# Performance work log

Hardware: AMD Instinct MI355X
Metric: run time of the kernel (lower is better)

The kernel has to match this reference:

```python
import jax, jax.numpy as jnp
import numpy as np

NUM_GRAPHS = 512
N_NODES = 100000
N_EDGES = 1600000
D_NODE = 128
D_EDGE = 32
D_OUT = 64


def setup_inputs() -> dict:
    key = jax.random.key(0)
    k = jax.random.split(key, 6)
    x = jax.random.normal(k[0], (N_NODES, D_NODE), dtype=jnp.float32)
    edge_index = jax.random.randint(k[1], (2, N_EDGES), 0, N_NODES, dtype=jnp.int64)
    edge_attr = jax.random.normal(k[2], (N_EDGES, D_EDGE), dtype=jnp.float32)
    u = jax.random.normal(k[3], (NUM_GRAPHS, D_OUT), dtype=jnp.float32)
    batch = jnp.sort(jax.random.randint(k[4], (N_NODES,), 0, NUM_GRAPHS, dtype=jnp.int64))
    W = jax.random.normal(k[5], (D_NODE + D_EDGE, D_OUT), dtype=jnp.float32) * 0.05
    b = jnp.full((D_OUT,), 0.01, dtype=jnp.float32)
    return {"x": x, "edge_index": edge_index, "edge_attr": edge_attr, "u": u, "batch": batch, "W": W, "b": b}


def reference(x, edge_index, edge_attr, u, batch, W, b):
    # row, col = edge_index; only col is used
    col = edge_index[1]
    # scatter_add nodes by graph id -> [B, D_NODE]
    node_aggregate = jax.ops.segment_sum(x, batch, num_segments=NUM_GRAPHS)
    # scatter_add edges by graph id of target node -> [B, D_EDGE]
    edge_aggregate = jax.ops.segment_sum(edge_attr, batch[col], num_segments=NUM_GRAPHS)
    out = jnp.concatenate([node_aggregate, edge_aggregate], axis=1)  # [B, 160]
    return out @ W + b  # [B, 64]
```

## Files before the change

### kernel.cpp

```cpp
#include <hip/hip_runtime.h>

#define NUM_GRAPHS 512
#define N_NODES 100000
#define N_EDGES 1600000
#define D_NODE 128
#define D_EDGE 32
#define D_OUT 64

#define NBLK 512
#define EPB (N_EDGES / NBLK)
#define GCAP 5120

__global__ __launch_bounds__(512) void count_kernel(const int* __restrict__ col,
                                                    const int* __restrict__ batch,
                                                    int* __restrict__ eg,
                                                    int* __restrict__ cntT) {
    __shared__ int cur[NUM_GRAPHS];
    const int t = threadIdx.x, b = blockIdx.x;
    cur[t] = 0;
    __syncthreads();
    const int base = b * EPB;

    int c[6], gg[6];
    #pragma unroll
    for (int r = 0; r < 6; ++r) c[r] = col[base + r * 512 + t];
    #pragma unroll
    for (int r = 0; r < 6; ++r) gg[r] = batch[c[r]];
    #pragma unroll
    for (int r = 0; r < 6; ++r) {
        eg[base + r * 512 + t] = gg[r];
        atomicAdd(&cur[gg[r]], 1);
    }
    if (t < EPB - 3072) {
        const int g = batch[col[base + 3072 + t]];
        eg[base + 3072 + t] = g;
        atomicAdd(&cur[g], 1);
    }
    __syncthreads();
    cntT[t * NBLK + b] = cur[t];
}

__global__ __launch_bounds__(512) void scan_kernel(const int* __restrict__ cntT,
                                                   int* __restrict__ pos,
                                                   int* __restrict__ totals) {
    const int g = blockIdx.x, t = threadIdx.x;
    const int n = cntT[g * NBLK + t];
    const int lane = t & 63, w = t >> 6;
    __shared__ int wtot[8], wbase[8];
    int v = n;
    #pragma unroll
    for (int off = 1; off < 64; off <<= 1) {
        const int u = __shfl_up(v, off, 64);
        if (lane >= off) v += u;
    }
    if (lane == 63) wtot[w] = v;
    __syncthreads();
    if (t == 0) {
        int s = 0;
        #pragma unroll
        for (int i = 0; i < 8; ++i) { wbase[i] = s; s += wtot[i]; }
    }
    __syncthreads();
    pos[t * NUM_GRAPHS + g] = g * GCAP + wbase[w] + v - n;
    if (t == 511) totals[g] = wbase[7] + v;
}

__global__ __launch_bounds__(512) void place_kernel(const int* __restrict__ eg,
                                                    const int* __restrict__ pos,
                                                    int* __restrict__ bucket) {
    __shared__ int cur[NUM_GRAPHS];
    const int t = threadIdx.x, b = blockIdx.x;
    cur[t] = pos[b * NUM_GRAPHS + t];
    __syncthreads();
    const int base = b * EPB;
    #pragma unroll
    for (int r = 0; r < 6; ++r) {
        const int i = r * 512 + t;
        const int g = eg[base + i];
        const int s = atomicAdd(&cur[g], 1);
        bucket[s] = base + i;
    }
    if (t < EPB - 3072) {
        const int i = 3072 + t;
        const int g = eg[base + i];
        bucket[atomicAdd(&cur[g], 1)] = base + i;
    }
}

__global__ __launch_bounds__(1024) void fused_kernel(const float* __restrict__ x,
                                                     const int* __restrict__ batch,
                                                     const float* __restrict__ edge_attr,
                                                     const int* __restrict__ totals,
                                                     const int* __restrict__ bucket,
                                                     const float* __restrict__ W,
                                                     const float* __restrict__ bias,
                                                     float* __restrict__ out) {
    const int g = blockIdx.x;
    const int t = threadIdx.x;
    __shared__ float4 red[1024];
    __shared__ float4 red2[64];
    __shared__ __align__(16) float feat[D_NODE + D_EDGE];

    const int ntot = min(totals[g], GCAP);
    const int* brow = bucket + g * GCAP;

    int l = 0, r = N_NODES;
    while (l < r) { int m = (l + r) >> 1; if (batch[m] < g) l = m + 1; else r = m; }
    const int lo = l;
    r = N_NODES;
    while (l < r) { int m = (l + r) >> 1; if (batch[m] < g + 1) l = m + 1; else r = m; }
    const int hi = l;

    const float4* x4 = reinterpret_cast<const float4*>(x);
    const int d4 = t & 31, rr = t >> 5;
    float4 a = make_float4(0.f, 0.f, 0.f, 0.f);
    for (int i = lo + rr; i < hi; i += 32) {
        const float4 v = x4[(size_t)i * 32 + d4];
        a.x += v.x; a.y += v.y; a.z += v.z; a.w += v.w;
    }
    red[t] = a;
    __syncthreads();
    if (t < 32) {
        float4 s = red[t];
        #pragma unroll
        for (int p = 1; p < 32; ++p) {
            const float4 u = red[p * 32 + t];
            s.x += u.x; s.y += u.y; s.z += u.z; s.w += u.w;
        }
        reinterpret_cast<float4*>(feat)[t] = s;
    }
    __syncthreads();

    const float4* ea4 = reinterpret_cast<const float4*>(edge_attr);
    const int slot0 = t >> 3, dq = t & 7;
    float4 a0 = make_float4(0.f, 0.f, 0.f, 0.f);
    float4 a1 = make_float4(0.f, 0.f, 0.f, 0.f);
    float4 a2 = make_float4(0.f, 0.f, 0.f, 0.f);
    float4 a3 = make_float4(0.f, 0.f, 0.f, 0.f);
    for (int base = 0; base < ntot; base += 512) {
        const int s0 = base + slot0, s1 = s0 + 128, s2 = s0 + 256, s3 = s0 + 384;
        const int id0 = (s0 < ntot) ? brow[s0] : -1;
        const int id1 = (s1 < ntot) ? brow[s1] : -1;
        const int id2 = (s2 < ntot) ? brow[s2] : -1;
        const int id3 = (s3 < ntot) ? brow[s3] : -1;
        if (id0 >= 0) { const float4 u = ea4[(size_t)id0 * 8 + dq]; a0.x += u.x; a0.y += u.y; a0.z += u.z; a0.w += u.w; }
        if (id1 >= 0) { const float4 u = ea4[(size_t)id1 * 8 + dq]; a1.x += u.x; a1.y += u.y; a1.z += u.z; a1.w += u.w; }
        if (id2 >= 0) { const float4 u = ea4[(size_t)id2 * 8 + dq]; a2.x += u.x; a2.y += u.y; a2.z += u.z; a2.w += u.w; }
        if (id3 >= 0) { const float4 u = ea4[(size_t)id3 * 8 + dq]; a3.x += u.x; a3.y += u.y; a3.z += u.z; a3.w += u.w; }
    }
    a0.x += a1.x + a2.x + a3.x;
    a0.y += a1.y + a2.y + a3.y;
    a0.z += a1.z + a2.z + a3.z;
    a0.w += a1.w + a2.w + a3.w;
    red[t] = a0;
    __syncthreads();
    if (t < 64) {
        const int part = t >> 3, dq2 = t & 7;
        float4 s = make_float4(0.f, 0.f, 0.f, 0.f);
        #pragma unroll
        for (int k = 0; k < 16; ++k) {
            const float4 u = red[(part * 16 + k) * 8 + dq2];
            s.x += u.x; s.y += u.y; s.z += u.z; s.w += u.w;
        }
        red2[t] = s;
    }
    __syncthreads();
    if (t < 8) {
        float4 s = red2[t];
        #pragma unroll
        for (int k = 1; k < 8; ++k) {
            const float4 u = red2[k * 8 + t];
            s.x += u.x; s.y += u.y; s.z += u.z; s.w += u.w;
        }
        reinterpret_cast<float4*>(feat + D_NODE)[t] = s;
    }
    __syncthreads();

    if (t < D_OUT) {
        float o = bias[t];
        #pragma unroll 8
        for (int k = 0; k < D_NODE + D_EDGE; ++k)
            o += feat[k] * W[k * D_OUT + t];
        out[g * D_OUT + t] = o;
    }
}

extern "C" void kernel_launch(void* const* d_in, const int* in_sizes, int n_in,
                              void* d_out, int out_size, void* d_ws, size_t ws_size,
                              hipStream_t stream) {
    const float* x          = (const float*)d_in[0];
    const int*   edge_index = (const int*)d_in[1];
    const float* edge_attr  = (const float*)d_in[2];
    const int*   batch      = (const int*)d_in[4];
    const float* W          = (const float*)d_in[5];
    const float* b          = (const float*)d_in[6];
    float* out = (float*)d_out;

    const int* col = edge_index + N_EDGES;

    int* eg     = (int*)d_ws;
    int* cntT   = eg + N_EDGES;
    int* pos    = cntT + NUM_GRAPHS * NBLK;
    int* totals = pos + NBLK * NUM_GRAPHS;
    int* bucket = totals + NUM_GRAPHS;

    count_kernel<<<NBLK, 512, 0, stream>>>(col, batch, eg, cntT);
    scan_kernel<<<NUM_GRAPHS, 512, 0, stream>>>(cntT, pos, totals);
    place_kernel<<<NBLK, 512, 0, stream>>>(eg, pos, bucket);
    fused_kernel<<<NUM_GRAPHS, 1024, 0, stream>>>(x, batch, edge_attr, totals, bucket, W, b, out);
}
```

Baseline: 83.71 us.

## Merge count, scan and place into one cooperative kernel with grid syncs

Replaces the count, scan and place launches with a single cooperative kernel that uses grid-wide syncs, and keeps each edge's graph id in registers so the eg array is never written or re-read. The node segment-sum moves into the middle phase, with each block reducing a contiguous node chunk and adding into node_agg through global atomics. The final kernel then only reads the precomputed node aggregate. This removes launch gaps and the eg round-trip, but adds grid-sync overhead, float atomics whose summation order can vary, and a requirement that all 512 blocks are co-resident.

```diff
diff --git a/kernel.cpp b/kernel.cpp
--- a/kernel.cpp
+++ b/kernel.cpp
@@ -1,4 +1,6 @@
 #include <hip/hip_runtime.h>
+#include <hip/hip_cooperative_groups.h>
+namespace cg = cooperative_groups;
 
 #define NUM_GRAPHS 512
 #define N_NODES 100000
@@ -9,89 +11,112 @@
 
 #define NBLK 512
 #define EPB (N_EDGES / NBLK)
+#define NREM (EPB - 3072)
 #define GCAP 5120
-
-__global__ __launch_bounds__(512) void count_kernel(const int* __restrict__ col,
-                                                    const int* __restrict__ batch,
-                                                    int* __restrict__ eg,
-                                                    int* __restrict__ cntT) {
+#define NCHUNK ((N_NODES + NBLK - 1) / NBLK)
+
+__global__ __launch_bounds__(512) void prep_kernel(const int* __restrict__ col,
+                                                   const int* __restrict__ batch,
+                                                   const float* __restrict__ x,
+                                                   int* __restrict__ cntT,
+                                                   int* __restrict__ pos,
+                                                   int* __restrict__ totals,
+                                                   int* __restrict__ bucket,
+                                                   float* __restrict__ node_agg) {
+    cg::grid_group grid = cg::this_grid();
+    const int t = threadIdx.x, b = blockIdx.x;
     __shared__ int cur[NUM_GRAPHS];
-    const int t = threadIdx.x, b = blockIdx.x;
+    __shared__ float4 red[512];
+    __shared__ int wtot[8], wbase[8];
+
     cur[t] = 0;
     __syncthreads();
     const int base = b * EPB;
-
-    int c[6], gg[6];
+    int c[6];
     #pragma unroll
     for (int r = 0; r < 6; ++r) c[r] = col[base + r * 512 + t];
+    const int crem = (t < NREM) ? col[base + 3072 + t] : 0;
+    int gg[6];
     #pragma unroll
     for (int r = 0; r < 6; ++r) gg[r] = batch[c[r]];
+    const int grem = (t < NREM) ? batch[crem] : -1;
+    #pragma unroll
+    for (int r = 0; r < 6; ++r) atomicAdd(&cur[gg[r]], 1);
+    if (grem >= 0) atomicAdd(&cur[grem], 1);
+    if (t < D_NODE) node_agg[b * D_NODE + t] = 0.f;
+    __syncthreads();
+    cntT[t * NBLK + b] = cur[t];
+    grid.sync();
+
+    {
+        const int n = cntT[b * NBLK + t];
+        const int lane = t & 63, w = t >> 6;
+        int v = n;
+        #pragma unroll
+        for (int off = 1; off < 64; off <<= 1) {
+            const int u = __shfl_up(v, off, 64);
+            if (lane >= off) v += u;
+        }
+        if (lane == 63) wtot[w] = v;
+        __syncthreads();
+        if (t == 0) {
+            int s = 0;
+            #pragma unroll
+            for (int i = 0; i < 8; ++i) { wbase[i] = s; s += wtot[i]; }
+        }
+        __syncthreads();
+        pos[t * NUM_GRAPHS + b] = b * GCAP + wbase[w] + v - n;
+        if (t == 511) totals[b] = wbase[7] + v;
+    }
+
+    {
+        const float4* x4 = reinterpret_cast<const float4*>(x);
+        const int d4 = t & 31, rr = t >> 5;
+        const int nbeg = b * NCHUNK;
+        const int nend = min(N_NODES, nbeg + NCHUNK);
+        int s = nbeg;
+        while (s < nend) {
+            const int gseg = batch[s];
+            int lo = s + 1, hi = nend;
+            while (lo < hi) { int m = (lo + hi) >> 1; if (batch[m] <= gseg) lo = m + 1; else hi = m; }
+            const int e = lo;
+            float4 a = make_float4(0.f, 0.f, 0.f, 0.f);
+            for (int i = s + rr; i < e; i += 16) {
+                const float4 u = x4[(size_t)i * 32 + d4];
+                a.x += u.x; a.y += u.y; a.z += u.z; a.w += u.w;
+            }
+            __syncthreads();
+            red[t] = a;
+            __syncthreads();
+            if (t < D_NODE) {
+                const int d4b = t >> 2, k = t & 3;
+                float v2 = 0.f;
+                #pragma unroll
+                for (int p = 0; p < 16; ++p) {
+                    const float4 u = red[p * 32 + d4b];
+                    v2 += (k == 0) ? u.x : (k == 1) ? u.y : (k == 2) ? u.z : u.w;
+                }
+                atomicAdd(&node_agg[gseg * D_NODE + t], v2);
+            }
+            s = e;
+        }
+    }
+    grid.sync();
+
+    cur[t] = pos[b * NUM_GRAPHS + t];
+    __syncthreads();
     #pragma unroll
     for (int r = 0; r < 6; ++r) {
-        eg[base + r * 512 + t] = gg[r];
-        atomicAdd(&cur[gg[r]], 1);
-    }
-    if (t < EPB - 3072) {
-        const int g = batch[col[base + 3072 + t]];
-        eg[base + 3072 + t] = g;
-        atomicAdd(&cur[g], 1);
-    }
-    __syncthreads();
-    cntT[t * NBLK + b] = cur[t];
+        const int s = atomicAdd(&cur[gg[r]], 1);
+        bucket[s] = base + r * 512 + t;
+    }
+    if (grem >= 0) bucket[atomicAdd(&cur[grem], 1)] = base + 3072 + t;
 }
 
-__global__ __launch_bounds__(512) void scan_kernel(const int* __restrict__ cntT,
-                                                   int* __restrict__ pos,
-                                                   int* __restrict__ totals) {
-    const int g = blockIdx.x, t = threadIdx.x;
-    const int n = cntT[g * NBLK + t];
-    const int lane = t & 63, w = t >> 6;
-    __shared__ int wtot[8], wbase[8];
-    int v = n;
-    #pragma unroll
-    for (int off = 1; off < 64; off <<= 1) {
-        const int u = __shfl_up(v, off, 64);
-        if (lane >= off) v += u;
-    }
-    if (lane == 63) wtot[w] = v;
-    __syncthreads();
-    if (t == 0) {
-        int s = 0;
-        #pragma unroll
-        for (int i = 0; i < 8; ++i) { wbase[i] = s; s += wtot[i]; }
-    }
-    __syncthreads();
-    pos[t * NUM_GRAPHS + g] = g * GCAP + wbase[w] + v - n;
-    if (t == 511) totals[g] = wbase[7] + v;
-}
-
-__global__ __launch_bounds__(512) void place_kernel(const int* __restrict__ eg,
-                                                    const int* __restrict__ pos,
-                                                    int* __restrict__ bucket) {
-    __shared__ int cur[NUM_GRAPHS];
-    const int t = threadIdx.x, b = blockIdx.x;
-    cur[t] = pos[b * NUM_GRAPHS + t];
-    __syncthreads();
-    const int base = b * EPB;
-    #pragma unroll
-    for (int r = 0; r < 6; ++r) {
-        const int i = r * 512 + t;
-        const int g = eg[base + i];
-        const int s = atomicAdd(&cur[g], 1);
-        bucket[s] = base + i;
-    }
-    if (t < EPB - 3072) {
-        const int i = 3072 + t;
-        const int g = eg[base + i];
-        bucket[atomicAdd(&cur[g], 1)] = base + i;
-    }
-}
-
-__global__ __launch_bounds__(1024) void fused_kernel(const float* __restrict__ x,
-                                                     const int* __restrict__ batch,
-                                                     const float* __restrict__ edge_attr,
+__global__ __launch_bounds__(1024) void fused_kernel(const float* __restrict__ edge_attr,
                                                      const int* __restrict__ totals,
                                                      const int* __restrict__ bucket,
+                                                     const float* __restrict__ node_agg,
                                                      const float* __restrict__ W,
                                                      const float* __restrict__ bias,
                                                      float* __restrict__ out) {
@@ -103,33 +128,9 @@
 
     const int ntot = min(totals[g], GCAP);
     const int* brow = bucket + g * GCAP;
-
-    int l = 0, r = N_NODES;
-    while (l < r) { int m = (l + r) >> 1; if (batch[m] < g) l = m + 1; else r = m; }
-    const int lo = l;
-    r = N_NODES;
-    while (l < r) { int m = (l + r) >> 1; if (batch[m] < g + 1) l = m + 1; else r = m; }
-    const int hi = l;
-
-    const float4* x4 = reinterpret_cast<const float4*>(x);
-    const int d4 = t & 31, rr = t >> 5;
-    float4 a = make_float4(0.f, 0.f, 0.f, 0.f);
-    for (int i = lo + rr; i < hi; i += 32) {
-        const float4 v = x4[(size_t)i * 32 + d4];
-        a.x += v.x; a.y += v.y; a.z += v.z; a.w += v.w;
-    }
-    red[t] = a;
-    __syncthreads();
-    if (t < 32) {
-        float4 s = red[t];
-        #pragma unroll
-        for (int p = 1; p < 32; ++p) {
-            const float4 u = red[p * 32 + t];
-            s.x += u.x; s.y += u.y; s.z += u.z; s.w += u.w;
-        }
-        reinterpret_cast<float4*>(feat)[t] = s;
-    }
-    __syncthreads();
+    if (t < 32)
+        reinterpret_cast<float4*>(feat)[t] =
+            reinterpret_cast<const float4*>(node_agg)[g * 32 + t];
 
     const float4* ea4 = reinterpret_cast<const float4*>(edge_attr);
     const int slot0 = t >> 3, dq = t & 7;
@@ -198,14 +199,16 @@
 
     const int* col = edge_index + N_EDGES;
 
-    int* eg     = (int*)d_ws;
-    int* cntT   = eg + N_EDGES;
-    int* pos    = cntT + NUM_GRAPHS * NBLK;
-    int* totals = pos + NBLK * NUM_GRAPHS;
-    int* bucket = totals + NUM_GRAPHS;
-
-    count_kernel<<<NBLK, 512, 0, stream>>>(col, batch, eg, cntT);
-    scan_kernel<<<NUM_GRAPHS, 512, 0, stream>>>(cntT, pos, totals);
-    place_kernel<<<NBLK, 512, 0, stream>>>(eg, pos, bucket);
-    fused_kernel<<<NUM_GRAPHS, 1024, 0, stream>>>(x, batch, edge_attr, totals, bucket, W, b, out);
+    int*   cntT     = (int*)d_ws;
+    int*   pos      = cntT + NUM_GRAPHS * NBLK;
+    int*   totals   = pos + NBLK * NUM_GRAPHS;
+    int*   bucket   = totals + NUM_GRAPHS;
+    float* node_agg = (float*)(bucket + (size_t)NUM_GRAPHS * GCAP);
+
+    void* args[] = {(void*)&col, (void*)&batch, (void*)&x, (void*)&cntT,
+                    (void*)&pos, (void*)&totals, (void*)&bucket, (void*)&node_agg};
+    hipLaunchCooperativeKernel((const void*)prep_kernel, dim3(NBLK), dim3(512),
+                               args, 0, stream);
+    fused_kernel<<<NUM_GRAPHS, 1024, 0, stream>>>(edge_attr, totals, bucket,
+                                                  node_agg, W, b, out);
 }
```

After: 197.6 us. 2.36x slower.

## Move node segment-sum into count kernel to overlap with edge gather latency

Applied to the files above, without the earlier changes.

The per-graph node feature reduction moves out of the final kernel and into the count kernel. Each block sums a contiguous 196-node chunk split by graph boundary, handling up to three segments, and writes partial sums that the final kernel adds up. This hides the x streaming behind the count kernel's dependent col/batch loads and shortens the final kernel. The edge gather loop is also widened from 4 to 8 outstanding loads per thread. The risk is silently dropping nodes if a chunk ever spans more than three graphs, and the extra registers used by the wider gather.

```diff
diff --git a/kernel.cpp b/kernel.cpp
--- a/kernel.cpp
+++ b/kernel.cpp
@@ -9,32 +9,71 @@
 
 #define NBLK 512
 #define EPB (N_EDGES / NBLK)
+#define NREM (EPB - 3072)
 #define GCAP 5120
+#define NCHUNK 196
+#define MAXSEG 3
 
 __global__ __launch_bounds__(512) void count_kernel(const int* __restrict__ col,
                                                     const int* __restrict__ batch,
+                                                    const float* __restrict__ x,
                                                     int* __restrict__ eg,
-                                                    int* __restrict__ cntT) {
+                                                    int* __restrict__ cntT,
+                                                    float* __restrict__ node_part) {
     __shared__ int cur[NUM_GRAPHS];
+    __shared__ float4 red[512];
     const int t = threadIdx.x, b = blockIdx.x;
     cur[t] = 0;
     __syncthreads();
     const int base = b * EPB;
 
-    int c[6], gg[6];
+    int c[6];
     #pragma unroll
     for (int r = 0; r < 6; ++r) c[r] = col[base + r * 512 + t];
+    const int crem = (t < NREM) ? col[base + 3072 + t] : 0;
+    int gg[6];
     #pragma unroll
     for (int r = 0; r < 6; ++r) gg[r] = batch[c[r]];
+    const int grem = (t < NREM) ? batch[crem] : -1;
+
+    const int nb = b * NCHUNK, ne = min(N_NODES, nb + NCHUNK);
+    const float4* x4 = reinterpret_cast<const float4*>(x);
+    const int d4 = t & 31, rr = t >> 5;
+    int s = nb, seg = 0;
+    while (s < ne && seg < MAXSEG) {
+        const int gseg = batch[s];
+        int lo = s + 1, hi = ne;
+        while (lo < hi) { int m = (lo + hi) >> 1; if (batch[m] <= gseg) lo = m + 1; else hi = m; }
+        const int e = lo;
+        float4 a = make_float4(0.f, 0.f, 0.f, 0.f);
+        for (int i = s + rr; i < e; i += 16) {
+            const float4 u = x4[(size_t)i * 32 + d4];
+            a.x += u.x; a.y += u.y; a.z += u.z; a.w += u.w;
+        }
+        red[t] = a;
+        __syncthreads();
+        if (t < D_NODE) {
+            const int d4b = t >> 2, k = t & 3;
+            float v = 0.f;
+            #pragma unroll
+            for (int p = 0; p < 16; ++p) {
+                const float4 u = red[p * 32 + d4b];
+                v += (k == 0) ? u.x : (k == 1) ? u.y : (k == 2) ? u.z : u.w;
+            }
+            node_part[((size_t)b * MAXSEG + seg) * D_NODE + t] = v;
+        }
+        __syncthreads();
+        ++seg; s = e;
+    }
+
     #pragma unroll
     for (int r = 0; r < 6; ++r) {
         eg[base + r * 512 + t] = gg[r];
         atomicAdd(&cur[gg[r]], 1);
     }
-    if (t < EPB - 3072) {
-        const int g = batch[col[base + 3072 + t]];
-        eg[base + 3072 + t] = g;
-        atomicAdd(&cur[g], 1);
+    if (grem >= 0) {
+        eg[base + 3072 + t] = grem;
+        atomicAdd(&cur[grem], 1);
     }
     __syncthreads();
     cntT[t * NBLK + b] = cur[t];
@@ -80,18 +119,18 @@
         const int s = atomicAdd(&cur[g], 1);
         bucket[s] = base + i;
     }
-    if (t < EPB - 3072) {
+    if (t < NREM) {
         const int i = 3072 + t;
         const int g = eg[base + i];
         bucket[atomicAdd(&cur[g], 1)] = base + i;
     }
 }
 
-__global__ __launch_bounds__(1024) void fused_kernel(const float* __restrict__ x,
+__global__ __launch_bounds__(1024) void fused_kernel(const float* __restrict__ edge_attr,
                                                      const int* __restrict__ batch,
-                                                     const float* __restrict__ edge_attr,
                                                      const int* __restrict__ totals,
                                                      const int* __restrict__ bucket,
+                                                     const float* __restrict__ node_part,
                                                      const float* __restrict__ W,
                                                      const float* __restrict__ bias,
                                                      float* __restrict__ out) {
@@ -110,49 +149,50 @@
     r = N_NODES;
     while (l < r) { int m = (l + r) >> 1; if (batch[m] < g + 1) l = m + 1; else r = m; }
     const int hi = l;
-
-    const float4* x4 = reinterpret_cast<const float4*>(x);
-    const int d4 = t & 31, rr = t >> 5;
-    float4 a = make_float4(0.f, 0.f, 0.f, 0.f);
-    for (int i = lo + rr; i < hi; i += 32) {
-        const float4 v = x4[(size_t)i * 32 + d4];
-        a.x += v.x; a.y += v.y; a.z += v.z; a.w += v.w;
-    }
-    red[t] = a;
-    __syncthreads();
-    if (t < 32) {
-        float4 s = red[t];
-        #pragma unroll
-        for (int p = 1; p < 32; ++p) {
-            const float4 u = red[p * 32 + t];
-            s.x += u.x; s.y += u.y; s.z += u.z; s.w += u.w;
-        }
-        reinterpret_cast<float4*>(feat)[t] = s;
-    }
-    __syncthreads();
+    if (t < D_NODE) {
+        float nv = 0.f;
+        if (lo < hi) {
+            const int cb0 = lo / NCHUNK, cb1 = (hi - 1) / NCHUNK;
+            for (int cb = cb0; cb <= cb1; ++cb) {
+                const int sg = g - batch[cb * NCHUNK];
+                if (sg >= 0 && sg < MAXSEG)
+                    nv += node_part[((size_t)cb * MAXSEG + sg) * D_NODE + t];
+            }
+        }
+        feat[t] = nv;
+    }
 
     const float4* ea4 = reinterpret_cast<const float4*>(edge_attr);
     const int slot0 = t >> 3, dq = t & 7;
-    float4 a0 = make_float4(0.f, 0.f, 0.f, 0.f);
-    float4 a1 = make_float4(0.f, 0.f, 0.f, 0.f);
-    float4 a2 = make_float4(0.f, 0.f, 0.f, 0.f);
-    float4 a3 = make_float4(0.f, 0.f, 0.f, 0.f);
-    for (int base = 0; base < ntot; base += 512) {
-        const int s0 = base + slot0, s1 = s0 + 128, s2 = s0 + 256, s3 = s0 + 384;
-        const int id0 = (s0 < ntot) ? brow[s0] : -1;
-        const int id1 = (s1 < ntot) ? brow[s1] : -1;
-        const int id2 = (s2 < ntot) ? brow[s2] : -1;
-        const int id3 = (s3 < ntot) ? brow[s3] : -1;
-        if (id0 >= 0) { const float4 u = ea4[(size_t)id0 * 8 + dq]; a0.x += u.x; a0.y += u.y; a0.z += u.z; a0.w += u.w; }
-        if (id1 >= 0) { const float4 u = ea4[(size_t)id1 * 8 + dq]; a1.x += u.x; a1.y += u.y; a1.z += u.z; a1.w += u.w; }
-        if (id2 >= 0) { const float4 u = ea4[(size_t)id2 * 8 + dq]; a2.x += u.x; a2.y += u.y; a2.z += u.z; a2.w += u.w; }
-        if (id3 >= 0) { const float4 u = ea4[(size_t)id3 * 8 + dq]; a3.x += u.x; a3.y += u.y; a3.z += u.z; a3.w += u.w; }
-    }
-    a0.x += a1.x + a2.x + a3.x;
-    a0.y += a1.y + a2.y + a3.y;
-    a0.z += a1.z + a2.z + a3.z;
-    a0.w += a1.w + a2.w + a3.w;
-    red[t] = a0;
+    float4 acc0 = make_float4(0.f,0.f,0.f,0.f), acc1 = acc0, acc2 = acc0, acc3 = acc0;
+    float4 acc4 = acc0, acc5 = acc0, acc6 = acc0, acc7 = acc0;
+    for (int base = 0; base < ntot; base += 1024) {
+        int id[8];
+        #pragma unroll
+        for (int k = 0; k < 8; ++k) {
+            const int s = base + slot0 + k * 128;
+            id[k] = (s < ntot) ? brow[s] : -1;
+        }
+        #pragma unroll
+        for (int k = 0; k < 8; ++k) {
+            if (id[k] >= 0) {
+                const float4 u = ea4[(size_t)id[k] * 8 + dq];
+                if (k == 0) { acc0.x+=u.x; acc0.y+=u.y; acc0.z+=u.z; acc0.w+=u.w; }
+                if (k == 1) { acc1.x+=u.x; acc1.y+=u.y; acc1.z+=u.z; acc1.w+=u.w; }
+                if (k == 2) { acc2.x+=u.x; acc2.y+=u.y; acc2.z+=u.z; acc2.w+=u.w; }
+                if (k == 3) { acc3.x+=u.x; acc3.y+=u.y; acc3.z+=u.z; acc3.w+=u.w; }
+                if (k == 4) { acc4.x+=u.x; acc4.y+=u.y; acc4.z+=u.z; acc4.w+=u.w; }
+                if (k == 5) { acc5.x+=u.x; acc5.y+=u.y; acc5.z+=u.z; acc5.w+=u.w; }
+                if (k == 6) { acc6.x+=u.x; acc6.y+=u.y; acc6.z+=u.z; acc6.w+=u.w; }
+                if (k == 7) { acc7.x+=u.x; acc7.y+=u.y; acc7.z+=u.z; acc7.w+=u.w; }
+            }
+        }
+    }
+    acc0.x += acc1.x + acc2.x + acc3.x + acc4.x + acc5.x + acc6.x + acc7.x;
+    acc0.y += acc1.y + acc2.y + acc3.y + acc4.y + acc5.y + acc6.y + acc7.y;
+    acc0.z += acc1.z + acc2.z + acc3.z + acc4.z + acc5.z + acc6.z + acc7.z;
+    acc0.w += acc1.w + acc2.w + acc3.w + acc4.w + acc5.w + acc6.w + acc7.w;
+    red[t] = acc0;
     __syncthreads();
     if (t < 64) {
         const int part = t >> 3, dq2 = t & 7;
@@ -198,14 +238,16 @@
 
     const int* col = edge_index + N_EDGES;
 
-    int* eg     = (int*)d_ws;
-    int* cntT   = eg + N_EDGES;
-    int* pos    = cntT + NUM_GRAPHS * NBLK;
-    int* totals = pos + NBLK * NUM_GRAPHS;
-    int* bucket = totals + NUM_GRAPHS;
-
-    count_kernel<<<NBLK, 512, 0, stream>>>(col, batch, eg, cntT);
+    int*   eg        = (int*)d_ws;
+    int*   cntT      = eg + N_EDGES;
+    int*   pos       = cntT + NUM_GRAPHS * NBLK;
+    int*   totals    = pos + NBLK * NUM_GRAPHS;
+    int*   bucket    = totals + NUM_GRAPHS;
+    float* node_part = (float*)(bucket + (size_t)NUM_GRAPHS * GCAP);
+
+    count_kernel<<<NBLK, 512, 0, stream>>>(col, batch, x, eg, cntT, node_part);
     scan_kernel<<<NUM_GRAPHS, 512, 0, stream>>>(cntT, pos, totals);
     place_kernel<<<NBLK, 512, 0, stream>>>(eg, pos, bucket);
-    fused_kernel<<<NUM_GRAPHS, 1024, 0, stream>>>(x, batch, edge_attr, totals, bucket, W, b, out);
-}
+    fused_kernel<<<NUM_GRAPHS, 1024, 0, stream>>>(edge_attr, batch, totals, bucket,
+                                                  node_part, W, b, out);
+}
```

Measured after the change: 89.67 us. 1.07x slower.
